# Performance work log

Measured on AMD Instinct MI355X. Metric: run time of the kernel, lower is better.

The kernel has to match this reference:

```python
import jax, jax.numpy as jnp
import numpy as np


def setup_inputs() -> dict:
    key = jax.random.key(0)
    k1, k2, k3, k4 = jax.random.split(key, 4)
    B, S, d_in, d_out = 4, 2048, 1024, 1024
    scale = 1.0 / np.sqrt(d_in)
    x = jax.random.normal(k1, (B, S, d_in), dtype=jnp.float32)
    # Linear weights stored as [d_in, d_out] so projection is x @ W
    Wq = jax.random.normal(k2, (d_in, d_out), dtype=jnp.float32) * scale
    Wk = jax.random.normal(k3, (d_in, d_out), dtype=jnp.float32) * scale
    Wv = jax.random.normal(k4, (d_in, d_out), dtype=jnp.float32) * scale
    return {"x": x, "Wq": Wq, "Wk": Wk, "Wv": Wv}


def reference(x, Wq, Wk, Wv):
    # QKV projections (no bias, matching qkv_bias=False)
    q = jnp.einsum("bsi,io->bso", x, Wq)
    k = jnp.einsum("bsi,io->bso", x, Wk)
    v = jnp.einsum("bsi,io->bso", x, Wv)
    d_k = k.shape[-1]
    # attn_scores = q @ k^T, causal mask (strict upper triangle -> -inf)
    scores = jnp.einsum("bqd,bkd->bqk", q, k)
    S = scores.shape[-1]
    causal = jnp.tril(jnp.ones((S, S), dtype=bool))  # True where allowed
    scores = jnp.where(causal, scores, -jnp.inf)
    attn = jax.nn.softmax(scores / jnp.sqrt(jnp.asarray(d_k, scores.dtype)), axis=-1)
    # dropout p=0.0 -> identity
    return jnp.einsum("bqk,bkd->bqd", attn, v)
```

## Files before the change

### kernel.cpp

```cpp
#include <hip/hip_runtime.h>

typedef _Float16 half8 __attribute__((ext_vector_type(8)));
typedef _Float16 half4 __attribute__((ext_vector_type(4)));
typedef float f32x4 __attribute__((ext_vector_type(4)));

#define ATT_SCALE 0.03125f
#define S_LEN 2048
#define D_DIM 1024
#define NB 4

__device__ __forceinline__ void async_cp16(const _Float16* g, _Float16* l)
{
    __builtin_amdgcn_global_load_lds(
        (const __attribute__((address_space(1))) void*)g,
        (__attribute__((address_space(3))) void*)l, 16, 0, 0);
}

__device__ __forceinline__ void gemm_core64(const _Float16* __restrict__ Ag,
                                            const _Float16* __restrict__ Bg,
                                            int lda, int ldb, int ksteps64,
                                            f32x4 acc[4][4])
{
    __shared__ _Float16 As[128 * 64];
    __shared__ _Float16 Bs[128 * 64];

    const int t    = threadIdx.x;
    const int wave = t >> 6;
    const int lane = t & 63;
    const int wm   = (wave >> 1) * 64;
    const int wn   = (wave & 1) * 64;
    const int lg   = lane >> 4;
    const int lr   = lane & 15;

    const int tr = t >> 3;
    const int tc = ((t & 7) ^ (tr & 7)) * 8;
    const int ldso = wave * 512;

    const _Float16* ap0 = Ag + (long)(0 * 32 + tr) * lda + tc;
    const _Float16* ap1 = Ag + (long)(1 * 32 + tr) * lda + tc;
    const _Float16* ap2 = Ag + (long)(2 * 32 + tr) * lda + tc;
    const _Float16* ap3 = Ag + (long)(3 * 32 + tr) * lda + tc;
    const _Float16* bp0 = Bg + (long)(0 * 32 + tr) * ldb + tc;
    const _Float16* bp1 = Bg + (long)(1 * 32 + tr) * ldb + tc;
    const _Float16* bp2 = Bg + (long)(2 * 32 + tr) * ldb + tc;
    const _Float16* bp3 = Bg + (long)(3 * 32 + tr) * ldb + tc;

    const int arow = wm + lr;
    const int brow = wn + lr;

    for (int ks = 0; ks < ksteps64; ++ks) {
        __syncthreads();
        async_cp16(ap0, As + 0 * 2048 + ldso);
        async_cp16(ap1, As + 1 * 2048 + ldso);
        async_cp16(ap2, As + 2 * 2048 + ldso);
        async_cp16(ap3, As + 3 * 2048 + ldso);
        async_cp16(bp0, Bs + 0 * 2048 + ldso);
        async_cp16(bp1, Bs + 1 * 2048 + ldso);
        async_cp16(bp2, Bs + 2 * 2048 + ldso);
        async_cp16(bp3, Bs + 3 * 2048 + ldso);
        __syncthreads();

        ap0 += 64; ap1 += 64; ap2 += 64; ap3 += 64;
        bp0 += 64; bp1 += 64; bp2 += 64; bp3 += 64;

#pragma unroll
        for (int kk = 0; kk < 2; ++kk) {
            half8 af[4], bf[4];
#pragma unroll
            for (int mf = 0; mf < 4; ++mf) {
                const int row = arow + mf * 16;
                const int hof = (kk * 32 + lg * 8) ^ ((row & 7) * 8);
                af[mf] = *(const half8*)&As[row * 64 + hof];
            }
#pragma unroll
            for (int nf = 0; nf < 4; ++nf) {
                const int row = brow + nf * 16;
                const int hof = (kk * 32 + lg * 8) ^ ((row & 7) * 8);
                bf[nf] = *(const half8*)&Bs[row * 64 + hof];
            }
#pragma unroll
            for (int mf = 0; mf < 4; ++mf)
#pragma unroll
                for (int nf = 0; nf < 4; ++nf)
                    acc[mf][nf] = __builtin_amdgcn_mfma_f32_16x16x32_f16(
                        af[mf], bf[nf], acc[mf][nf], 0, 0, 0);
        }
    }
}

__global__ void init_kernel(const float* __restrict__ X, _Float16* __restrict__ Xh,
                            float* __restrict__ rs,
                            const float* __restrict__ Wq, const float* __restrict__ Wk,
                            const float* __restrict__ Wv, _Float16* __restrict__ Wt)
{
    const int bid = blockIdx.x;
    const int t   = threadIdx.x;
    if (bid < 8192) {
        const int i = bid * 256 + t;
        float4 v = ((const float4*)X)[i];
        half4 h;
        h.x = (_Float16)v.x; h.y = (_Float16)v.y; h.z = (_Float16)v.z; h.w = (_Float16)v.w;
        ((half4*)Xh)[i] = h;
        if (i < NB * S_LEN) rs[i] = 0.f;
        return;
    }
    __shared__ float tile[32][33];
    const int bb = bid - 8192;
    const int w  = bb >> 10;
    const int rem = bb & 1023;
    const int n0 = (rem & 31) * 32, k0 = (rem >> 5) * 32;
    const float* Wsrc = (w == 0) ? Wq : (w == 1) ? Wk : Wv;
    _Float16* dst = Wt + (long)w * D_DIM * D_DIM;
    const int tx = t & 31, ty = t >> 5;
#pragma unroll
    for (int j = 0; j < 4; ++j)
        tile[ty + 8 * j][tx] = Wsrc[(long)(k0 + ty + 8 * j) * D_DIM + n0 + tx];
    __syncthreads();
#pragma unroll
    for (int j = 0; j < 4; ++j)
        dst[(long)(n0 + ty + 8 * j) * D_DIM + k0 + tx] = (_Float16)tile[tx][ty + 8 * j];
}

__global__ __launch_bounds__(256) void proj_kernel(const _Float16* __restrict__ Xh,
                                                   const _Float16* __restrict__ Wt,
                                                   _Float16* __restrict__ Q,
                                                   _Float16* __restrict__ K,
                                                   _Float16* __restrict__ V)
{
    const int flat = blockIdx.x;
    const int swz  = (flat & 7) * 192 + (flat >> 3);
    const int nt = swz & 7, mt = (swz >> 3) & 63, w = swz >> 9;

    f32x4 acc[4][4];
#pragma unroll
    for (int i = 0; i < 4; ++i)
#pragma unroll
        for (int j = 0; j < 4; ++j) acc[i][j] = (f32x4){0.f, 0.f, 0.f, 0.f};

    const _Float16* Ag = Xh + (long)mt * 128 * D_DIM;
    const _Float16* Bg = Wt + (long)w * D_DIM * D_DIM + (long)nt * 128 * D_DIM;
    gemm_core64(Ag, Bg, D_DIM, D_DIM, D_DIM / 64, acc);

    _Float16* C = (w == 0) ? Q : (w == 1) ? K : V;
    const int t = threadIdx.x, wave = t >> 6, lane = t & 63;
    const int wm = (wave >> 1) * 64, wn = (wave & 1) * 64;
    const int lg = lane >> 4, lr = lane & 15;
    const long row0 = (long)mt * 128 + wm + 4 * lg;
    const long col0 = (long)nt * 128 + wn + lr;
#pragma unroll
    for (int i = 0; i < 4; ++i)
#pragma unroll
        for (int j = 0; j < 4; ++j)
#pragma unroll
            for (int r = 0; r < 4; ++r)
                C[(row0 + i * 16 + r) * D_DIM + col0 + j * 16] = (_Float16)acc[i][j][r];
}

__global__ __launch_bounds__(256) void scores_tv_kernel(const _Float16* __restrict__ Q,
                                                        const _Float16* __restrict__ K,
                                                        const _Float16* __restrict__ V,
                                                        _Float16* __restrict__ P,
                                                        float* __restrict__ row_sum,
                                                        _Float16* __restrict__ Vt)
{
    __shared__ _Float16 ttile[64][72];
    if (blockIdx.x >= 544) {
        const int tv = blockIdx.x - 544;
        const int d0 = (tv & 15) * 64;
        const int s0 = ((tv >> 4) & 31) * 64;
        const long b = tv >> 9;
        const _Float16* Vb = V + b * S_LEN * D_DIM;
        _Float16* Vtb = Vt + b * D_DIM * S_LEN;
        const int t = threadIdx.x;
        const int sr = t >> 3, c8 = (t & 7) * 8;

        *(half8*)&ttile[sr][c8]      = *(const half8*)&Vb[(long)(s0 + sr) * D_DIM + d0 + c8];
        *(half8*)&ttile[sr + 32][c8] = *(const half8*)&Vb[(long)(s0 + sr + 32) * D_DIM + d0 + c8];
        __syncthreads();

        const int dr = t >> 3, s8 = (t & 7) * 8;
        half8 o0, o1;
#pragma unroll
        for (int e = 0; e < 8; ++e) {
            o0[e] = ttile[s8 + e][dr];
            o1[e] = ttile[s8 + e][dr + 32];
        }
        *(half8*)&Vtb[(long)(d0 + dr) * S_LEN + s0 + s8]      = o0;
        *(half8*)&Vtb[(long)(d0 + dr + 32) * S_LEN + s0 + s8] = o1;
        return;
    }

    const int xcd = blockIdx.x & 7;
    const int idx = blockIdx.x >> 3;
    const int b   = idx / 17;
    const int l   = idx % 17;
    int qt, kt;
    if (l <= xcd) { qt = xcd;      kt = l; }
    else          { qt = 15 - xcd; kt = l - xcd - 1; }

    f32x4 acc[4][4];
#pragma unroll
    for (int i = 0; i < 4; ++i)
#pragma unroll
        for (int j = 0; j < 4; ++j) acc[i][j] = (f32x4){0.f, 0.f, 0.f, 0.f};

    const _Float16* Ag = Q + ((long)b * S_LEN + qt * 128) * D_DIM;
    const _Float16* Bg = K + ((long)b * S_LEN + kt * 128) * D_DIM;
    gemm_core64(Ag, Bg, D_DIM, D_DIM, D_DIM / 64, acc);

    _Float16* Pb = P + (long)b * S_LEN * S_LEN;
    float* rsb = row_sum + (long)b * S_LEN;
    const int t = threadIdx.x, wave = t >> 6, lane = t & 63;
    const int wm = (wave >> 1) * 64, wn = (wave & 1) * 64;
    const int lg = lane >> 4, lr = lane & 15;
    const int row0 = qt * 128 + wm + 4 * lg;
    const int col0 = kt * 128 + wn + lr;

#pragma unroll
    for (int i = 0; i < 4; ++i) {
#pragma unroll
        for (int r = 0; r < 4; ++r) {
            const int row = row0 + i * 16 + r;
            float s = 0.f;
#pragma unroll
            for (int j = 0; j < 4; ++j) {
                const int col = col0 + j * 16;
                float p = (col <= row) ? __expf(acc[i][r * 0 + j][r] * 0.f + acc[i][j][r] * ATT_SCALE) : 0.f;
                s += p;
                Pb[(long)row * S_LEN + col] = (_Float16)p;
            }
#pragma unroll
            for (int off = 1; off < 16; off <<= 1) s += __shfl_xor(s, off, 64);
            if (lr == 0) atomicAdd(&rsb[row], s);
        }
    }
}

__global__ __launch_bounds__(256) void pv_kernel(const _Float16* __restrict__ P,
                                                 const _Float16* __restrict__ Vt,
                                                 const float* __restrict__ row_sum,
                                                 float* __restrict__ O)
{
    const int idx = blockIdx.x;
    const int qt  = 15 - (idx >> 5);
    const int rem = idx & 31;
    const int nt  = rem >> 2;
    const int b   = rem & 3;

    const int ks64 = (qt + 1) * 2;

    f32x4 acc[4][4];
#pragma unroll
    for (int i = 0; i < 4; ++i)
#pragma unroll
        for (int jj = 0; jj < 4; ++jj) acc[i][jj] = (f32x4){0.f, 0.f, 0.f, 0.f};

    const _Float16* Ag = P + ((long)b * S_LEN + qt * 128) * S_LEN;
    const _Float16* Bg = Vt + (long)b * D_DIM * S_LEN + (long)nt * 128 * S_LEN;
    gemm_core64(Ag, Bg, S_LEN, S_LEN, ks64, acc);

    float* Ob = O + (long)b * S_LEN * D_DIM;
    const float* rsb = row_sum + (long)b * S_LEN;
    const int t = threadIdx.x, wave = t >> 6, lane = t & 63;
    const int wm = (wave >> 1) * 64, wn = (wave & 1) * 64;
    const int lg = lane >> 4, lr = lane & 15;
    const long row0 = qt * 128 + wm + 4 * lg;
    const long col0 = (long)nt * 128 + wn + lr;

#pragma unroll
    for (int i = 0; i < 4; ++i)
#pragma unroll
        for (int rr = 0; rr < 4; ++rr) {
            const float inv = 1.f / rsb[row0 + i * 16 + rr];
#pragma unroll
            for (int jj = 0; jj < 4; ++jj)
                Ob[(row0 + i * 16 + rr) * D_DIM + col0 + jj * 16] = acc[i][jj][rr] * inv;
        }
}

extern "C" void kernel_launch(void* const* d_in, const int* in_sizes, int n_in,
                              void* d_out, int out_size, void* d_ws, size_t ws_size,
                              hipStream_t stream)
{
    const float* x  = (const float*)d_in[0];
    const float* Wq = (const float*)d_in[1];
    const float* Wk = (const float*)d_in[2];
    const float* Wv = (const float*)d_in[3];
    float* out = (float*)d_out;

    char* ws = (char*)d_ws;
    const long MiB = 1024 * 1024;
    _Float16* Q  = (_Float16*)(ws + 0 * MiB);
    _Float16* K  = (_Float16*)(ws + 16 * MiB);
    _Float16* V  = (_Float16*)(ws + 32 * MiB);
    _Float16* Vt = (_Float16*)(ws + 48 * MiB);
    _Float16* Xh = (_Float16*)(ws + 64 * MiB);
    _Float16* Wt = (_Float16*)(ws + 80 * MiB);
    _Float16* P  = (_Float16*)(ws + 86 * MiB);
    float*    RS = (float*)   (ws + 118 * MiB);

    init_kernel<<<dim3(8192 + 3072), dim3(256), 0, stream>>>(x, Xh, RS, Wq, Wk, Wv, Wt);
    proj_kernel<<<dim3(1536), dim3(256), 0, stream>>>(Xh, Wt, Q, K, V);
    scores_tv_kernel<<<dim3(2592), dim3(256), 0, stream>>>(Q, K, V, P, RS, Vt);
    pv_kernel<<<dim3(512), dim3(256), 0, stream>>>(P, Vt, RS, out);
}
```

Before: 155.1 us.

## Fuse V transpose into projection epilogue via shared-memory staging

The V projection blocks now stage their accumulator tile in shared memory with an XOR swizzle and write V transposed directly, so the separate V buffer and the transpose blocks in the scores kernel are gone. The scores kernel launches only the 544 QK^T tiles. This removes one full write and read of V in exchange for an extra LDS round trip and barriers in a third of the projection blocks. A dead multiply-by-zero term in the exp is also dropped.

New measurement: 157.4 us. About the same (+1.5%).

```diff
diff --git a/kernel.cpp b/kernel.cpp
--- a/kernel.cpp
+++ b/kernel.cpp
@@ -16,13 +16,14 @@
         (__attribute__((address_space(3))) void*)l, 16, 0, 0);
 }
 
-__device__ __forceinline__ void gemm_core64(const _Float16* __restrict__ Ag,
+__device__ __forceinline__ void gemm_core64(_Float16* __restrict__ smem,
+                                            const _Float16* __restrict__ Ag,
                                             const _Float16* __restrict__ Bg,
                                             int lda, int ldb, int ksteps64,
                                             f32x4 acc[4][4])
 {
-    __shared__ _Float16 As[128 * 64];
-    __shared__ _Float16 Bs[128 * 64];
+    _Float16* As = smem;
+    _Float16* Bs = smem + 8192;
 
     const int t    = threadIdx.x;
     const int wave = t >> 6;
@@ -125,8 +126,10 @@
                                                    const _Float16* __restrict__ Wt,
                                                    _Float16* __restrict__ Q,
                                                    _Float16* __restrict__ K,
-                                                   _Float16* __restrict__ V)
-{
+                                                   _Float16* __restrict__ Vt)
+{
+    __shared__ _Float16 smem[16384];
+
     const int flat = blockIdx.x;
     const int swz  = (flat & 7) * 192 + (flat >> 3);
     const int nt = swz & 7, mt = (swz >> 3) & 63, w = swz >> 9;
@@ -139,56 +142,71 @@
 
     const _Float16* Ag = Xh + (long)mt * 128 * D_DIM;
     const _Float16* Bg = Wt + (long)w * D_DIM * D_DIM + (long)nt * 128 * D_DIM;
-    gemm_core64(Ag, Bg, D_DIM, D_DIM, D_DIM / 64, acc);
-
-    _Float16* C = (w == 0) ? Q : (w == 1) ? K : V;
+    gemm_core64(smem, Ag, Bg, D_DIM, D_DIM, D_DIM / 64, acc);
+
     const int t = threadIdx.x, wave = t >> 6, lane = t & 63;
     const int wm = (wave >> 1) * 64, wn = (wave & 1) * 64;
     const int lg = lane >> 4, lr = lane & 15;
-    const long row0 = (long)mt * 128 + wm + 4 * lg;
-    const long col0 = (long)nt * 128 + wn + lr;
-#pragma unroll
-    for (int i = 0; i < 4; ++i)
-#pragma unroll
-        for (int j = 0; j < 4; ++j)
-#pragma unroll
-            for (int r = 0; r < 4; ++r)
-                C[(row0 + i * 16 + r) * D_DIM + col0 + j * 16] = (_Float16)acc[i][j][r];
-}
-
-__global__ __launch_bounds__(256) void scores_tv_kernel(const _Float16* __restrict__ Q,
-                                                        const _Float16* __restrict__ K,
-                                                        const _Float16* __restrict__ V,
-                                                        _Float16* __restrict__ P,
-                                                        float* __restrict__ row_sum,
-                                                        _Float16* __restrict__ Vt)
-{
-    __shared__ _Float16 ttile[64][72];
-    if (blockIdx.x >= 544) {
-        const int tv = blockIdx.x - 544;
-        const int d0 = (tv & 15) * 64;
-        const int s0 = ((tv >> 4) & 31) * 64;
-        const long b = tv >> 9;
-        const _Float16* Vb = V + b * S_LEN * D_DIM;
-        _Float16* Vtb = Vt + b * D_DIM * S_LEN;
-        const int t = threadIdx.x;
-        const int sr = t >> 3, c8 = (t & 7) * 8;
-
-        *(half8*)&ttile[sr][c8]      = *(const half8*)&Vb[(long)(s0 + sr) * D_DIM + d0 + c8];
-        *(half8*)&ttile[sr + 32][c8] = *(const half8*)&Vb[(long)(s0 + sr + 32) * D_DIM + d0 + c8];
-        __syncthreads();
-
-        const int dr = t >> 3, s8 = (t & 7) * 8;
-        half8 o0, o1;
-#pragma unroll
-        for (int e = 0; e < 8; ++e) {
-            o0[e] = ttile[s8 + e][dr];
-            o1[e] = ttile[s8 + e][dr + 32];
+
+    if (w < 2) {
+        _Float16* C = (w == 0) ? Q : K;
+        const long row0 = (long)mt * 128 + wm + 4 * lg;
+        const long col0 = (long)nt * 128 + wn + lr;
+#pragma unroll
+        for (int i = 0; i < 4; ++i)
+#pragma unroll
+            for (int j = 0; j < 4; ++j)
+#pragma unroll
+                for (int r = 0; r < 4; ++r)
+                    C[(row0 + i * 16 + r) * D_DIM + col0 + j * 16] = (_Float16)acc[i][j][r];
+        return;
+    }
+
+    __syncthreads();
+    {
+        const int srow0 = wm + 4 * lg;
+        const int scol0 = wn + lr;
+#pragma unroll
+        for (int i = 0; i < 4; ++i)
+#pragma unroll
+            for (int r = 0; r < 4; ++r) {
+                const int srow = srow0 + i * 16 + r;
+                const int cs = ((srow >> 2) & 7) << 4;
+#pragma unroll
+                for (int j = 0; j < 4; ++j)
+                    smem[srow * 128 + ((scol0 + j * 16) ^ cs)] = (_Float16)acc[i][j][r];
+            }
+    }
+    __syncthreads();
+
+    const int b     = mt >> 4;
+    const int sbase = (mt & 15) * 128;
+    _Float16* Vtb = Vt + (long)b * D_DIM * S_LEN + (long)nt * 128 * S_LEN;
+    const int dr8 = t >> 3;
+    const int s8  = (t & 7) * 8;
+#pragma unroll
+    for (int dblk = 0; dblk < 4; ++dblk) {
+        const int dl = dblk * 32 + dr8;
+#pragma unroll
+        for (int sh = 0; sh < 2; ++sh) {
+            const int sl = sh * 64 + s8;
+            half8 o;
+#pragma unroll
+            for (int e = 0; e < 8; ++e) {
+                const int s = sl + e;
+                o[e] = smem[s * 128 + (dl ^ (((s >> 2) & 7) << 4))];
+            }
+            *(half8*)&Vtb[(long)dl * S_LEN + sbase + sl] = o;
         }
-        *(half8*)&Vtb[(long)(d0 + dr) * S_LEN + s0 + s8]      = o0;
-        *(half8*)&Vtb[(long)(d0 + dr + 32) * S_LEN + s0 + s8] = o1;
-        return;
-    }
+    }
+}
+
+__global__ __launch_bounds__(256) void scores_exp_kernel(const _Float16* __restrict__ Q,
+                                                         const _Float16* __restrict__ K,
+                                                         _Float16* __restrict__ P,
+                                                         float* __restrict__ row_sum)
+{
+    __shared__ _Float16 smem[16384];
 
     const int xcd = blockIdx.x & 7;
     const int idx = blockIdx.x >> 3;
@@ -206,7 +224,7 @@
 
     const _Float16* Ag = Q + ((long)b * S_LEN + qt * 128) * D_DIM;
     const _Float16* Bg = K + ((long)b * S_LEN + kt * 128) * D_DIM;
-    gemm_core64(Ag, Bg, D_DIM, D_DIM, D_DIM / 64, acc);
+    gemm_core64(smem, Ag, Bg, D_DIM, D_DIM, D_DIM / 64, acc);
 
     _Float16* Pb = P + (long)b * S_LEN * S_LEN;
     float* rsb = row_sum + (long)b * S_LEN;
@@ -225,7 +243,7 @@
 #pragma unroll
             for (int j = 0; j < 4; ++j) {
                 const int col = col0 + j * 16;
-                float p = (col <= row) ? __expf(acc[i][r * 0 + j][r] * 0.f + acc[i][j][r] * ATT_SCALE) : 0.f;
+                float p = (col <= row) ? __expf(acc[i][j][r] * ATT_SCALE) : 0.f;
                 s += p;
                 Pb[(long)row * S_LEN + col] = (_Float16)p;
             }
@@ -241,6 +259,8 @@
                                                  const float* __restrict__ row_sum,
                                                  float* __restrict__ O)
 {
+    __shared__ _Float16 smem[16384];
+
     const int idx = blockIdx.x;
     const int qt  = 15 - (idx >> 5);
     const int rem = idx & 31;
@@ -257,7 +277,7 @@
 
     const _Float16* Ag = P + ((long)b * S_LEN + qt * 128) * S_LEN;
     const _Float16* Bg = Vt + (long)b * D_DIM * S_LEN + (long)nt * 128 * S_LEN;
-    gemm_core64(Ag, Bg, S_LEN, S_LEN, ks64, acc);
+    gemm_core64(smem, Ag, Bg, S_LEN, S_LEN, ks64, acc);
 
     float* Ob = O + (long)b * S_LEN * D_DIM;
     const float* rsb = row_sum + (long)b * S_LEN;
@@ -292,7 +312,6 @@
     const long MiB = 1024 * 1024;
     _Float16* Q  = (_Float16*)(ws + 0 * MiB);
     _Float16* K  = (_Float16*)(ws + 16 * MiB);
-    _Float16* V  = (_Float16*)(ws + 32 * MiB);
     _Float16* Vt = (_Float16*)(ws + 48 * MiB);
     _Float16* Xh = (_Float16*)(ws + 64 * MiB);
     _Float16* Wt = (_Float16*)(ws + 80 * MiB);
@@ -300,7 +319,7 @@
     float*    RS = (float*)   (ws + 118 * MiB);
 
     init_kernel<<<dim3(8192 + 3072), dim3(256), 0, stream>>>(x, Xh, RS, Wq, Wk, Wv, Wt);
-    proj_kernel<<<dim3(1536), dim3(256), 0, stream>>>(Xh, Wt, Q, K, V);
-    scores_tv_kernel<<<dim3(2592), dim3(256), 0, stream>>>(Q, K, V, P, RS, Vt);
+    proj_kernel<<<dim3(1536), dim3(256), 0, stream>>>(Xh, Wt, Q, K, Vt);
+    scores_exp_kernel<<<dim3(544), dim3(256), 0, stream>>>(Q, K, P, RS);
     pv_kernel<<<dim3(512), dim3(256), 0, stream>>>(P, Vt, RS, out);
 }
```
